# Performance work log

Hardware: AMD Instinct MI355X
Metric: run time of the kernel (lower is better)

Reference implementation:

```python
import jax, jax.numpy as jnp
import numpy as np

B, H, S, D = 4, 16, 2048, 64

def setup_inputs() -> dict:
    key = jax.random.key(0)
    kq, kk, kv = jax.random.split(key, 3)
    q = jax.random.normal(kq, (B, H, S, D), dtype=jnp.float32)
    k = jax.random.normal(kk, (B, H, S, D), dtype=jnp.float32)
    v = jax.random.normal(kv, (B, H, S, D), dtype=jnp.float32)
    return {"q": q, "k": k, "v": v}

def reference(q, k, v):
    # naive unfused attention: scores = QK^T / sqrt(d), softmax, then @ V
    scale = 1.0 / jnp.sqrt(jnp.asarray(q.shape[-1], q.dtype))
    scores = jnp.einsum('bhqd,bhkd->bhqk', q, k) * scale  # [B,H,S,S] materialized
    attn = jax.nn.softmax(scores, axis=-1)
    out = jnp.einsum('bhqk,bhkd->bhqd', attn, v)
    return out
```

## Files before the change

### kernel.cpp

```cpp
#include <hip/hip_runtime.h>


#define S_LEN 2048
#define D_DIM 64
#define N_BH  64
#define QSCALE 0.18033688011112042f

typedef _Float16 half8 __attribute__((ext_vector_type(8)));
typedef _Float16 half4 __attribute__((ext_vector_type(4)));
typedef float floatx16 __attribute__((ext_vector_type(16)));
typedef unsigned int uint4v __attribute__((ext_vector_type(4)));

#define MFMA32(a, b, c) __builtin_amdgcn_mfma_f32_32x32x16_f16((a), (b), (c), 0, 0, 0)

__global__ __launch_bounds__(256) void prep_kernel(
    const float* __restrict__ kg, const float* __restrict__ vg,
    _Float16* __restrict__ kh, _Float16* __restrict__ vt)
{
    __shared__ _Float16 Ls[64][72];
    const int tid = threadIdx.x;
    const int bh = blockIdx.y;
    const int sbase = blockIdx.x * 64;
    const size_t gbase = ((size_t)(bh * S_LEN + sbase)) * D_DIM;

#pragma unroll
    for (int i = 0; i < 4; ++i) {
        const int e = i * 1024 + tid * 4;
        const int s = e >> 6, d0 = e & 63;
        const float4 kv = *(const float4*)(kg + gbase + e);
        half4 hk;
        hk[0] = (_Float16)kv.x; hk[1] = (_Float16)kv.y;
        hk[2] = (_Float16)kv.z; hk[3] = (_Float16)kv.w;
        *(half4*)(kh + gbase + e) = hk;
        const float4 vv = *(const float4*)(vg + gbase + e);
        Ls[d0 + 0][s] = (_Float16)vv.x;
        Ls[d0 + 1][s] = (_Float16)vv.y;
        Ls[d0 + 2][s] = (_Float16)vv.z;
        Ls[d0 + 3][s] = (_Float16)vv.w;
    }
    __syncthreads();
    const int d = tid >> 2, c = tid & 3;
    _Float16* dst = vt + ((size_t)bh * D_DIM + d) * S_LEN + sbase + c * 16;
    *(half8*)(dst)     = *(const half8*)&Ls[d][c * 16];
    *(half8*)(dst + 8) = *(const half8*)&Ls[d][c * 16 + 8];
}

__global__ __launch_bounds__(256) void fa_kernel(
    const float* __restrict__ qg, const _Float16* __restrict__ kh,
    const _Float16* __restrict__ vt, float* __restrict__ outg)
{
    __shared__ _Float16 Kl[64 * 64];
    __shared__ _Float16 Vl[64 * 64];

    const int tid = threadIdx.x;
    const int w = tid >> 6;
    const int L = tid & 63;
    const int lq = L & 31;
    const int h = L >> 5;

    const int id = blockIdx.x;
    const int bh   = ((id & 7) << 3) | (id >> 7);
    const int qblk = (id >> 3) & 15;
    const int qrow = qblk * 128 + w * 32 + lq;

    half8 qb[4];
    {
        const float* qp = qg + ((size_t)bh * S_LEN + qrow) * D_DIM + h * 8;
#pragma unroll
        for (int ks = 0; ks < 4; ++ks) {
            const float4 a = *(const float4*)(qp + ks * 16);
            const float4 b = *(const float4*)(qp + ks * 16 + 4);
            qb[ks][0] = (_Float16)(a.x * QSCALE);
            qb[ks][1] = (_Float16)(a.y * QSCALE);
            qb[ks][2] = (_Float16)(a.z * QSCALE);
            qb[ks][3] = (_Float16)(a.w * QSCALE);
            qb[ks][4] = (_Float16)(b.x * QSCALE);
            qb[ks][5] = (_Float16)(b.y * QSCALE);
            qb[ks][6] = (_Float16)(b.z * QSCALE);
            qb[ks][7] = (_Float16)(b.w * QSCALE);
        }
    }

    floatx16 o0, o1, lac;
#pragma unroll
    for (int r = 0; r < 16; ++r) { o0[r] = 0.f; o1[r] = 0.f; lac[r] = 0.f; }

    half8 ones;
#pragma unroll
    for (int j = 0; j < 8; ++j) ones[j] = (_Float16)1.0f;

    const size_t kgbase = (size_t)bh * S_LEN * D_DIM;
    const size_t vgbase = (size_t)bh * D_DIM * S_LEN;

    for (int kt = 0; kt < S_LEN / 64; ++kt) {
        const int kbase = kt * 64;

#pragma unroll
        for (int i = 0; i < 2; ++i) {
            const int cid = i * 64 + L;
            const int row = w * 16 + (cid >> 3);
            const int c = cid & 7;
            const int sw = ((c ^ (row & 7)) << 3);
            *(half8*)&Kl[row * 64 + sw] =
                *(const half8*)(kh + kgbase + (size_t)(kbase + row) * D_DIM + c * 8);
            *(half8*)&Vl[row * 64 + sw] =
                *(const half8*)(vt + vgbase + (size_t)row * S_LEN + kbase + c * 8);
        }
        __syncthreads();

        floatx16 sa0, sa1;
#pragma unroll
        for (int r = 0; r < 16; ++r) { sa0[r] = 0.f; sa1[r] = 0.f; }
#pragma unroll
        for (int ks = 0; ks < 4; ++ks) {
            const int sw = (((2 * ks + h) ^ (lq & 7)) << 3);
            const half8 ka0 = *(const half8*)&Kl[lq * 64 + sw];
            const half8 ka1 = *(const half8*)&Kl[(32 + lq) * 64 + sw];
            sa0 = MFMA32(ka0, qb[ks], sa0);
            sa1 = MFMA32(ka1, qb[ks], sa1);
        }

        unsigned int pk0[8], pk1[8];
#pragma unroll
        for (int p = 0; p < 8; ++p) {
            const auto e0 = __builtin_amdgcn_cvt_pkrtz(
                __builtin_amdgcn_exp2f(sa0[2 * p]),
                __builtin_amdgcn_exp2f(sa0[2 * p + 1]));
            const auto e1 = __builtin_amdgcn_cvt_pkrtz(
                __builtin_amdgcn_exp2f(sa1[2 * p]),
                __builtin_amdgcn_exp2f(sa1[2 * p + 1]));
            pk0[p] = __builtin_bit_cast(unsigned int, e0);
            pk1[p] = __builtin_bit_cast(unsigned int, e1);
        }

#pragma unroll
        for (int mt = 0; mt < 2; ++mt) {
            const unsigned int* pk = mt ? pk1 : pk0;
            const unsigned int t0 = h ? pk[0] : pk[2];
            const unsigned int t1 = h ? pk[1] : pk[3];
            const unsigned int t2 = h ? pk[4] : pk[6];
            const unsigned int t3 = h ? pk[5] : pk[7];
            const unsigned int r0 = __shfl_xor(t0, 32, 64);
            const unsigned int r1 = __shfl_xor(t1, 32, 64);
            const unsigned int r2 = __shfl_xor(t2, 32, 64);
            const unsigned int r3 = __shfl_xor(t3, 32, 64);
            uint4v u0, u1;
            if (h == 0) {
                u0[0] = pk[0]; u0[1] = pk[1]; u0[2] = r0; u0[3] = r1;
                u1[0] = pk[4]; u1[1] = pk[5]; u1[2] = r2; u1[3] = r3;
            } else {
                u0[0] = r0; u0[1] = r1; u0[2] = pk[2]; u0[3] = pk[3];
                u1[0] = r2; u1[1] = r3; u1[2] = pk[6]; u1[3] = pk[7];
            }
            const half8 af0 = __builtin_bit_cast(half8, u0);
            const half8 af1 = __builtin_bit_cast(half8, u1);
#pragma unroll
            for (int kl = 0; kl < 2; ++kl) {
                const int ksg = mt * 2 + kl;
                const half8 af = kl ? af1 : af0;
                const int sw = (((2 * ksg + h) ^ (lq & 7)) << 3);
                const half8 vb0 = *(const half8*)&Vl[lq * 64 + sw];
                const half8 vb1 = *(const half8*)&Vl[(32 + lq) * 64 + sw];
                lac = MFMA32(af, ones, lac);
                o0 = MFMA32(af, vb0, o0);
                o1 = MFMA32(af, vb1, o1);
            }
        }
        __syncthreads();
    }

    float* ob = outg + ((size_t)bh * S_LEN + qblk * 128 + w * 32) * D_DIM;
#pragma unroll
    for (int reg = 0; reg < 16; ++reg) {
        const int q = (reg & 3) + 8 * (reg >> 2) + 4 * h;
        const float inv = 1.0f / lac[reg];
        ob[(size_t)q * D_DIM + lq]      = o0[reg] * inv;
        ob[(size_t)q * D_DIM + 32 + lq] = o1[reg] * inv;
    }
}

extern "C" void kernel_launch(void* const* d_in, const int* in_sizes, int n_in,
                              void* d_out, int out_size, void* d_ws, size_t ws_size,
                              hipStream_t stream) {
    const float* q = (const float*)d_in[0];
    const float* k = (const float*)d_in[1];
    const float* v = (const float*)d_in[2];
    float* out = (float*)d_out;
    (void)in_sizes; (void)n_in; (void)out_size; (void)ws_size;

    _Float16* kh = (_Float16*)d_ws;
    _Float16* vt = kh + (size_t)N_BH * S_LEN * D_DIM;

    prep_kernel<<<dim3(S_LEN / 64, N_BH), dim3(256), 0, stream>>>(k, v, kh, vt);
    fa_kernel<<<dim3(1024), dim3(256), 0, stream>>>(q, kh, vt, out);
}
```

Measured before the change: 222.7 us.

## Load K/V tiles via global_load_lds, halve workgroup size, swizzle prep LDS

The attention kernel now copies K and V tiles straight from global memory into LDS with the global_load_lds builtin instead of going through registers. Workgroups shrink from 4 to 2 waves covering 64 query rows, and the grid doubles to 2048 blocks. The prep kernel's padded transpose buffer is replaced by an XOR-swizzled unpadded layout. Each block now reloads K/V for fewer query rows, which doubles K/V traffic through LDS in exchange for lower register staging cost and possibly better occupancy and latency hiding.

```diff
diff --git a/kernel.cpp b/kernel.cpp
--- a/kernel.cpp
+++ b/kernel.cpp
@@ -13,11 +13,15 @@
 
 #define MFMA32(a, b, c) __builtin_amdgcn_mfma_f32_32x32x16_f16((a), (b), (c), 0, 0, 0)
 
+#define GLL16(g, l) __builtin_amdgcn_global_load_lds(                      \
+    (const __attribute__((address_space(1))) void*)(g),                    \
+    (__attribute__((address_space(3))) void*)(l), 16, 0, 0)
+
 __global__ __launch_bounds__(256) void prep_kernel(
     const float* __restrict__ kg, const float* __restrict__ vg,
     _Float16* __restrict__ kh, _Float16* __restrict__ vt)
 {
-    __shared__ _Float16 Ls[64][72];
+    __shared__ _Float16 Ls[64 * 64];
     const int tid = threadIdx.x;
     const int bh = blockIdx.y;
     const int sbase = blockIdx.x * 64;
@@ -33,19 +37,20 @@
         hk[2] = (_Float16)kv.z; hk[3] = (_Float16)kv.w;
         *(half4*)(kh + gbase + e) = hk;
         const float4 vv = *(const float4*)(vg + gbase + e);
-        Ls[d0 + 0][s] = (_Float16)vv.x;
-        Ls[d0 + 1][s] = (_Float16)vv.y;
-        Ls[d0 + 2][s] = (_Float16)vv.z;
-        Ls[d0 + 3][s] = (_Float16)vv.w;
+        const int base = ((((s >> 3) ^ ((d0 >> 2) & 7)) << 3) | (s & 7));
+        Ls[(d0 + 0) * 64 + base] = (_Float16)vv.x;
+        Ls[(d0 + 1) * 64 + base] = (_Float16)vv.y;
+        Ls[(d0 + 2) * 64 + base] = (_Float16)vv.z;
+        Ls[(d0 + 3) * 64 + base] = (_Float16)vv.w;
     }
     __syncthreads();
-    const int d = tid >> 2, c = tid & 3;
-    _Float16* dst = vt + ((size_t)bh * D_DIM + d) * S_LEN + sbase + c * 16;
-    *(half8*)(dst)     = *(const half8*)&Ls[d][c * 16];
-    *(half8*)(dst + 8) = *(const half8*)&Ls[d][c * 16 + 8];
+    const int d = tid >> 2, c = tid & 3, sw = (d >> 2) & 7;
+    _Float16* dst = vt + ((size_t)(bh * D_DIM + d)) * S_LEN + sbase + c * 16;
+    *(half8*)(dst)     = *(const half8*)&Ls[d * 64 + (((2 * c)     ^ sw) << 3)];
+    *(half8*)(dst + 8) = *(const half8*)&Ls[d * 64 + (((2 * c + 1) ^ sw) << 3)];
 }
 
-__global__ __launch_bounds__(256) void fa_kernel(
+__global__ __launch_bounds__(128) void fa_kernel(
     const float* __restrict__ qg, const _Float16* __restrict__ kh,
     const _Float16* __restrict__ vt, float* __restrict__ outg)
 {
@@ -59,9 +64,9 @@
     const int h = L >> 5;
 
     const int id = blockIdx.x;
-    const int bh   = ((id & 7) << 3) | (id >> 7);
-    const int qblk = (id >> 3) & 15;
-    const int qrow = qblk * 128 + w * 32 + lq;
+    const int bh   = ((id & 7) << 3) | (id >> 8);
+    const int qblk = (id >> 3) & 31;
+    const int qrow = qblk * 64 + w * 32 + lq;
 
     half8 qb[4];
     {
@@ -89,23 +94,24 @@
 #pragma unroll
     for (int j = 0; j < 8; ++j) ones[j] = (_Float16)1.0f;
 
-    const size_t kgbase = (size_t)bh * S_LEN * D_DIM;
-    const size_t vgbase = (size_t)bh * D_DIM * S_LEN;
+    const int rloc = L >> 3, lc = L & 7;
+    const int crd = lc ^ rloc;
+    const _Float16* kgl = kh + (size_t)bh * S_LEN * D_DIM
+                        + (size_t)(w * 32 + rloc) * D_DIM + crd * 8;
+    const _Float16* vgl = vt + (size_t)bh * D_DIM * S_LEN
+                        + (size_t)(w * 32 + rloc) * S_LEN + crd * 8;
+    _Float16* const kld = &Kl[w * 32 * 64];
+    _Float16* const vld = &Vl[w * 32 * 64];
 
     for (int kt = 0; kt < S_LEN / 64; ++kt) {
-        const int kbase = kt * 64;
-
-#pragma unroll
-        for (int i = 0; i < 2; ++i) {
-            const int cid = i * 64 + L;
-            const int row = w * 16 + (cid >> 3);
-            const int c = cid & 7;
-            const int sw = ((c ^ (row & 7)) << 3);
-            *(half8*)&Kl[row * 64 + sw] =
-                *(const half8*)(kh + kgbase + (size_t)(kbase + row) * D_DIM + c * 8);
-            *(half8*)&Vl[row * 64 + sw] =
-                *(const half8*)(vt + vgbase + (size_t)row * S_LEN + kbase + c * 8);
-        }
+        __syncthreads();
+#pragma unroll
+        for (int i = 0; i < 4; ++i) {
+            GLL16(kgl + (size_t)i * 8 * D_DIM, kld + i * 8 * 64);
+            GLL16(vgl + (size_t)i * 8 * S_LEN, vld + i * 8 * 64);
+        }
+        kgl += 64 * D_DIM;
+        vgl += 64;
         __syncthreads();
 
         floatx16 sa0, sa1;
@@ -166,10 +172,9 @@
                 o1 = MFMA32(af, vb1, o1);
             }
         }
-        __syncthreads();
-    }
-
-    float* ob = outg + ((size_t)bh * S_LEN + qblk * 128 + w * 32) * D_DIM;
+    }
+
+    float* ob = outg + ((size_t)bh * S_LEN + qblk * 64 + w * 32) * D_DIM;
 #pragma unroll
     for (int reg = 0; reg < 16; ++reg) {
         const int q = (reg & 3) + 8 * (reg >> 2) + 4 * h;
@@ -192,5 +197,5 @@
     _Float16* vt = kh + (size_t)N_BH * S_LEN * D_DIM;
 
     prep_kernel<<<dim3(S_LEN / 64, N_BH), dim3(256), 0, stream>>>(k, v, kh, vt);
-    fa_kernel<<<dim3(1024), dim3(256), 0, stream>>>(q, kh, vt, out);
+    fa_kernel<<<dim3(2048), dim3(128), 0, stream>>>(q, kh, vt, out);
 }
```

After: 246.5 us. 10.7% more time.
